# Kernel optimization log

Hardware: AMD Instinct MI355X
Metric: run time of the kernel (lower is better)

## Reference

```python
import jax, jax.numpy as jnp
import numpy as np

N_NODES = 100000


def gcn_conv(x, W, b, src, dst, n):
    """PyG GCNConv with default add_self_loops and symmetric normalization."""
    xw = x @ W  # [N, out]
    loop = jnp.arange(n, dtype=src.dtype)
    s = jnp.concatenate([src, loop])  # source j
    d = jnp.concatenate([dst, loop])  # target i
    deg = jax.ops.segment_sum(jnp.ones_like(d, dtype=xw.dtype), d, num_segments=n)
    dinv = jnp.where(deg > 0, jax.lax.rsqrt(deg), 0.0)
    norm = dinv[s] * dinv[d]  # [E+N]
    msg = xw[s] * norm[:, None]
    out = jax.ops.segment_sum(msg, d, num_segments=n)
    return out + b


def setup_inputs() -> dict:
    key = jax.random.key(0)
    ks = jax.random.split(key, 9)
    n, e, f = N_NODES, 1600000, 512
    x = jax.random.normal(ks[0], (n, f), dtype=jnp.float32)
    edge_index = jax.random.randint(ks[1], (2, e), 0, n, dtype=jnp.int32)
    y = jax.random.uniform(ks[2], (n, 1), dtype=jnp.float32)
    W1 = jax.random.normal(ks[3], (f, 64), dtype=jnp.float32) / np.sqrt(f)
    b1 = jnp.zeros((64,), jnp.float32)
    W2 = jax.random.normal(ks[4], (64, 256), dtype=jnp.float32) / np.sqrt(64)
    b2 = jnp.zeros((256,), jnp.float32)
    W3 = jax.random.normal(ks[5], (256, 1), dtype=jnp.float32) / np.sqrt(256)
    b3 = jnp.zeros((1,), jnp.float32)
    return {"x": x, "edge_index": edge_index, "y": y,
            "W1": W1, "b1": b1, "W2": W2, "b2": b2, "W3": W3, "b3": b3}


def reference(x, edge_index, y, W1, b1, W2, b2, W3, b3):
    n = x.shape[0]
    src, dst = edge_index[0], edge_index[1]
    h = jax.nn.relu(gcn_conv(x, W1, b1, src, dst, n))
    # dropout is identity in eval mode
    h = jax.nn.relu(gcn_conv(h, W2, b2, src, dst, n))
    z = gcn_conv(h, W3, b3, src, dst, n)  # logits [N, 1]
    # BCE(sigmoid(z), y), computed stably via log-sigmoid
    loss = -(y * jax.nn.log_sigmoid(z) + (1.0 - y) * jax.nn.log_sigmoid(-z))
    return jnp.mean(loss)
```

## Files before the change

kernel.cpp:

```cpp
#include <hip/hip_runtime.h>
#include <math.h>

typedef __attribute__((ext_vector_type(8))) short s16x8;
typedef __attribute__((ext_vector_type(4))) float f32x4;

__device__ inline ushort f2bf(float f) {
    union { float f; unsigned u; } v; v.f = f;
    unsigned r = v.u + 0x7FFF + ((v.u >> 16) & 1);
    return (ushort)(r >> 16);
}
__device__ inline float bf2f(ushort h) {
    union { unsigned u; float f; } v; v.u = ((unsigned)h) << 16;
    return v.f;
}
__device__ inline float bfLo(unsigned u) {
    union { unsigned x; float f; } v; v.x = u << 16; return v.f;
}
__device__ inline float bfHi(unsigned u) {
    union { unsigned x; float f; } v; v.x = u & 0xFFFF0000u; return v.f;
}


__global__ void hist_kernel(const int* __restrict__ dst, int E, int* __restrict__ cnt,
                            int* __restrict__ slot) {
    int e = blockIdx.x * blockDim.x + threadIdx.x;
    if (e < E) slot[e] = atomicAdd(&cnt[dst[e]], 1);
}

__global__ void alloc_kernel(const int* __restrict__ cnt, int* __restrict__ row_start,
                             float* __restrict__ dinv, int* __restrict__ total, int N) {
    int i = blockIdx.x * blockDim.x + threadIdx.x;
    int lane = threadIdx.x & 63;
    int c = (i < N) ? cnt[i] : 0;
    int inc = c;
#pragma unroll
    for (int o = 1; o < 64; o <<= 1) {
        int v = __shfl_up(inc, o, 64);
        if (lane >= o) inc += v;
    }
    int wsum = __shfl(inc, 63, 64);
    int base = 0;
    if (lane == 0) base = atomicAdd(total, wsum);
    base = __shfl(base, 0, 64);
    if (i < N) {
        row_start[i] = base + inc - c;
        dinv[i] = rsqrtf((float)(c + 1));
    }
}

__global__ void scatter_kernel(const int* __restrict__ src, const int* __restrict__ dst, int E,
                               const int* __restrict__ row_start, const int* __restrict__ slot,
                               int* __restrict__ csr) {
    int e = blockIdx.x * blockDim.x + threadIdx.x;
    if (e < E) {
        int d = dst[e];
        csr[row_start[d] + slot[e]] = src[e];
    }
}

__global__ void wsplit_all_kernel(const float* __restrict__ W1, const float* __restrict__ W2,
                                  ushort* __restrict__ wt_hi, ushort* __restrict__ wt_lo,
                                  ushort* __restrict__ wt2_hi, ushort* __restrict__ wt2_lo) {
    int idx = blockIdx.x * blockDim.x + threadIdx.x;
    if (idx < 64 * 512) {
        int n = idx & 63, k = idx >> 6;
        float f = W1[k * 64 + n];
        ushort h = f2bf(f);
        wt_hi[n * 512 + k] = h;
        wt_lo[n * 512 + k] = f2bf(f - bf2f(h));
    } else if (idx < 64 * 512 + 64 * 256) {
        int i2 = idx - 64 * 512;
        int n = i2 & 255, k = i2 >> 8;
        float f = W2[k * 256 + n];
        ushort h = f2bf(f);
        wt2_hi[n * 64 + k] = h;
        wt2_lo[n * 64 + k] = f2bf(f - bf2f(h));
    }
}

__global__ __launch_bounds__(256, 3) void gemm1_kernel(const float* __restrict__ x,
                                                       const ushort* __restrict__ wt_hi,
                                                       const ushort* __restrict__ wt_lo,
                                                       const float* __restrict__ dinv,
                                                       ushort* __restrict__ out, int N) {
    __shared__ __align__(16) short xs_hi[128 * 64];
    __shared__ __align__(16) short xs_lo[128 * 64];
    __shared__ __align__(16) short ws_hi[64 * 64];
    __shared__ __align__(16) short ws_lo[64 * 64];

    const int tid = threadIdx.x;
    const int nodeBase = blockIdx.x * 128;
    const int wave = tid >> 6, lane = tid & 63;
    const int m16 = lane & 15, quad = lane >> 4;

    f32x4 acc[2][4];
#pragma unroll
    for (int mt = 0; mt < 2; mt++)
#pragma unroll
        for (int nt = 0; nt < 4; nt++) acc[mt][nt] = (f32x4){0.f, 0.f, 0.f, 0.f};

    for (int kc = 0; kc < 512; kc += 64) {
        __syncthreads();
#pragma unroll
        for (int i = 0; i < 4; i++) {
            int f = tid + i * 256;
            int node = f >> 3, g = f & 7;
            int gn = nodeBase + node;
            if (gn >= N) gn = N - 1;
            const float4 a = *(const float4*)(x + (size_t)gn * 512 + kc + g * 8);
            const float4 b = *(const float4*)(x + (size_t)gn * 512 + kc + g * 8 + 4);
            float ff[8] = {a.x, a.y, a.z, a.w, b.x, b.y, b.z, b.w};
            union { ushort u[8]; uint4 v; } H, L;
#pragma unroll
            for (int j = 0; j < 8; j++) {
                ushort h = f2bf(ff[j]);
                H.u[j] = h;
                L.u[j] = f2bf(ff[j] - bf2f(h));
            }
            int gp = (g + node) & 7;
            *(uint4*)&xs_hi[node * 64 + gp * 8] = H.v;
            *(uint4*)&xs_lo[node * 64 + gp * 8] = L.v;
        }
#pragma unroll
        for (int i = 0; i < 2; i++) {
            int f = tid + i * 256;
            int n = f >> 3, g = f & 7;
            int gp = (g + n) & 7;
            *(uint4*)&ws_hi[n * 64 + gp * 8] =
                *(const uint4*)(wt_hi + (size_t)n * 512 + kc + g * 8);
            *(uint4*)&ws_lo[n * 64 + gp * 8] =
                *(const uint4*)(wt_lo + (size_t)n * 512 + kc + g * 8);
        }
        __syncthreads();
#pragma unroll
        for (int ck = 0; ck < 2; ck++) {
            s16x8 Ah[2], Al[2];
#pragma unroll
            for (int mt = 0; mt < 2; mt++) {
                int row = (wave * 2 + mt) * 16 + m16;
                int gp = (ck * 4 + quad + row) & 7;
                Ah[mt] = *(s16x8*)&xs_hi[row * 64 + gp * 8];
                Al[mt] = *(s16x8*)&xs_lo[row * 64 + gp * 8];
            }
#pragma unroll
            for (int nt = 0; nt < 4; nt++) {
                int n = nt * 16 + m16;
                int gp = (ck * 4 + quad + n) & 7;
                s16x8 Bh = *(s16x8*)&ws_hi[n * 64 + gp * 8];
                s16x8 Bl = *(s16x8*)&ws_lo[n * 64 + gp * 8];
#pragma unroll
                for (int mt = 0; mt < 2; mt++) {
                    acc[mt][nt] = __builtin_amdgcn_mfma_f32_16x16x32_bf16(Ah[mt], Bh, acc[mt][nt], 0, 0, 0);
                    acc[mt][nt] = __builtin_amdgcn_mfma_f32_16x16x32_bf16(Ah[mt], Bl, acc[mt][nt], 0, 0, 0);
                    acc[mt][nt] = __builtin_amdgcn_mfma_f32_16x16x32_bf16(Al[mt], Bh, acc[mt][nt], 0, 0, 0);
                }
            }
        }
    }
#pragma unroll
    for (int mt = 0; mt < 2; mt++) {
#pragma unroll
        for (int r = 0; r < 4; r++) {
            int gn = nodeBase + (wave * 2 + mt) * 16 + quad * 4 + r;
            if (gn < N) {
                float di = dinv[gn];
#pragma unroll
                for (int nt = 0; nt < 4; nt++)
                    out[(size_t)gn * 64 + nt * 16 + m16] = f2bf(di * acc[mt][nt][r]);
            }
        }
    }
}

template <int RELU, int BIAS, int PREMUL>
__global__ void agg64bf_kernel(const ushort* __restrict__ in, ushort* __restrict__ out,
                               const int* __restrict__ row_start, const int* __restrict__ cnt,
                               const int* __restrict__ csr, const float* __restrict__ dinv,
                               const float* __restrict__ bias, int N) {
    int gw = (int)((blockIdx.x * (size_t)blockDim.x + threadIdx.x) >> 6);
    int lane = threadIdx.x & 63;
    if (gw >= N) return;
    const int m16 = lane & 15;
    const int quad = lane >> 4;

    const int s = row_start[gw];
    const int c = cnt[gw];
    const int total = c + 1;

    float a0 = 0.f, a1 = 0.f, a2v = 0.f, a3 = 0.f;
    for (int e = 0; e < total; e += 8) {
        int s0 = e + quad, s1 = e + 4 + quad;
        bool v0 = s0 < total, v1 = s1 < total;
        int j0 = gw, j1 = gw;
        if (v0 && s0 > 0) j0 = csr[s + s0 - 1];
        if (v1 && s1 > 0) j1 = csr[s + s1 - 1];
        uint2 u0 = *(const uint2*)(in + (size_t)j0 * 64 + m16 * 4);
        uint2 u1 = *(const uint2*)(in + (size_t)j1 * 64 + m16 * 4);
        if (v0) { a0 += bfLo(u0.x); a1 += bfHi(u0.x); a2v += bfLo(u0.y); a3 += bfHi(u0.y); }
        if (v1) { a0 += bfLo(u1.x); a1 += bfHi(u1.x); a2v += bfLo(u1.y); a3 += bfHi(u1.y); }
    }
    a0 += __shfl_xor(a0, 16, 64); a0 += __shfl_xor(a0, 32, 64);
    a1 += __shfl_xor(a1, 16, 64); a1 += __shfl_xor(a1, 32, 64);
    a2v += __shfl_xor(a2v, 16, 64); a2v += __shfl_xor(a2v, 32, 64);
    a3 += __shfl_xor(a3, 16, 64); a3 += __shfl_xor(a3, 32, 64);

    float di = dinv[gw];
    float r0 = di * a0, r1 = di * a1, r2 = di * a2v, r3 = di * a3;
    if (BIAS) {
        float4 bv = *(const float4*)&bias[m16 * 4];
        r0 += bv.x; r1 += bv.y; r2 += bv.z; r3 += bv.w;
    }
    if (RELU) {
        r0 = fmaxf(r0, 0.f); r1 = fmaxf(r1, 0.f);
        r2 = fmaxf(r2, 0.f); r3 = fmaxf(r3, 0.f);
    }
    if (PREMUL) { r0 *= di; r1 *= di; r2 *= di; r3 *= di; }
    if (quad == 0) {
        uint2 o;
        o.x = ((unsigned)f2bf(r1) << 16) | f2bf(r0);
        o.y = ((unsigned)f2bf(r3) << 16) | f2bf(r2);
        *(uint2*)(out + (size_t)gw * 64 + m16 * 4) = o;
    }
}

__global__ __launch_bounds__(256, 2) void gemm23_kernel(const ushort* __restrict__ a2,
                                                        const ushort* __restrict__ wt2_hi,
                                                        const ushort* __restrict__ wt2_lo,
                                                        const float* __restrict__ b2,
                                                        const float* __restrict__ W3,
                                                        const float* __restrict__ dinv,
                                                        float* __restrict__ r, int N) {
    const int tid = threadIdx.x;
    const int wave = tid >> 6, lane = tid & 63;
    const int m16 = lane & 15, quad = lane >> 4;
    const int rowBase = blockIdx.x * 128 + wave * 32;

    s16x8 A[2][2];
#pragma unroll
    for (int mt = 0; mt < 2; mt++) {
        int gn = rowBase + mt * 16 + m16;
        if (gn >= N) gn = N - 1;
        const ushort* ap = a2 + (size_t)gn * 64 + quad * 8;
#pragma unroll
        for (int ck = 0; ck < 2; ck++)
            A[mt][ck] = *(const s16x8*)(ap + ck * 32);
    }

    f32x4 acc[2][16];
#pragma unroll
    for (int mt = 0; mt < 2; mt++)
#pragma unroll
        for (int nt = 0; nt < 16; nt++) acc[mt][nt] = (f32x4){0.f, 0.f, 0.f, 0.f};

#pragma unroll
    for (int nt = 0; nt < 16; nt++) {
        int n = nt * 16 + m16;
        const ushort* bh = wt2_hi + (size_t)n * 64 + quad * 8;
        const ushort* bl = wt2_lo + (size_t)n * 64 + quad * 8;
        s16x8 Bh0 = *(const s16x8*)(bh);
        s16x8 Bh1 = *(const s16x8*)(bh + 32);
        s16x8 Bl0 = *(const s16x8*)(bl);
        s16x8 Bl1 = *(const s16x8*)(bl + 32);
        acc[0][nt] = __builtin_amdgcn_mfma_f32_16x16x32_bf16(A[0][0], Bh0, acc[0][nt], 0, 0, 0);
        acc[1][nt] = __builtin_amdgcn_mfma_f32_16x16x32_bf16(A[1][0], Bh0, acc[1][nt], 0, 0, 0);
        acc[0][nt] = __builtin_amdgcn_mfma_f32_16x16x32_bf16(A[0][1], Bh1, acc[0][nt], 0, 0, 0);
        acc[1][nt] = __builtin_amdgcn_mfma_f32_16x16x32_bf16(A[1][1], Bh1, acc[1][nt], 0, 0, 0);
        acc[0][nt] = __builtin_amdgcn_mfma_f32_16x16x32_bf16(A[0][0], Bl0, acc[0][nt], 0, 0, 0);
        acc[1][nt] = __builtin_amdgcn_mfma_f32_16x16x32_bf16(A[1][0], Bl0, acc[1][nt], 0, 0, 0);
        acc[0][nt] = __builtin_amdgcn_mfma_f32_16x16x32_bf16(A[0][1], Bl1, acc[0][nt], 0, 0, 0);
        acc[1][nt] = __builtin_amdgcn_mfma_f32_16x16x32_bf16(A[1][1], Bl1, acc[1][nt], 0, 0, 0);
    }

    float bv[16], wv[16];
#pragma unroll
    for (int nt = 0; nt < 16; nt++) {
        bv[nt] = b2[nt * 16 + m16];
        wv[nt] = W3[nt * 16 + m16];
    }
#pragma unroll
    for (int mt = 0; mt < 2; mt++) {
#pragma unroll
        for (int rr = 0; rr < 4; rr++) {
            float p = 0.f;
#pragma unroll
            for (int nt = 0; nt < 16; nt++) {
                float v = fmaxf(acc[mt][nt][rr] + bv[nt], 0.f);
                p = fmaf(v, wv[nt], p);
            }
#pragma unroll
            for (int off = 1; off < 16; off <<= 1) p += __shfl_xor(p, off, 64);
            int gn = rowBase + mt * 16 + quad * 4 + rr;
            if (m16 == 0 && gn < N) r[gn] = dinv[gn] * p;
        }
    }
}

__global__ __launch_bounds__(1024) void loss_kernel(const float* __restrict__ r,
                                                    const float* __restrict__ dinv,
                                                    const int* __restrict__ row_start,
                                                    const int* __restrict__ cnt,
                                                    const int* __restrict__ csr,
                                                    const float* __restrict__ y,
                                                    const float* __restrict__ b3,
                                                    float* __restrict__ out,
                                                    int N, float invN) {
    const int lane = threadIdx.x & 63;
    const int wave = threadIdx.x >> 6;
    const int l16 = lane & 15;
    const int grp = lane >> 4;
    const int waveId = blockIdx.x * 16 + wave;
    const int nWaves = gridDim.x * 16;
    const float b3v = b3[0];

    float loss = 0.f;
    for (int base = waveId * 4; base < N; base += nWaves * 4) {
        int node = base + grp;
        float acc = 0.f;
        if (node < N) {
            int s = row_start[node], c = cnt[node];
            for (int e = l16; e < c; e += 16) acc += r[csr[s + e]];
        }
        acc += __shfl_xor(acc, 1, 64);
        acc += __shfl_xor(acc, 2, 64);
        acc += __shfl_xor(acc, 4, 64);
        acc += __shfl_xor(acc, 8, 64);
        if (node < N && l16 == 0) {
            float z = dinv[node] * (r[node] + acc) + b3v;
            float yv = y[node];
            float L = log1pf(expf(-fabsf(z)));
            float spz  = fmaxf(z, 0.f) + L;
            float spnz = fmaxf(-z, 0.f) + L;
            loss += yv * spnz + (1.f - yv) * spz;
        }
    }
#pragma unroll
    for (int off = 1; off < 64; off <<= 1) loss += __shfl_xor(loss, off, 64);
    __shared__ float red[16];
    if (lane == 0) red[wave] = loss;
    __syncthreads();
    if (threadIdx.x == 0) {
        float t = 0.f;
#pragma unroll
        for (int i = 0; i < 16; i++) t += red[i];
        atomicAdd(out, t * invN);
    }
}

extern "C" void kernel_launch(void* const* d_in, const int* in_sizes, int n_in,
                              void* d_out, int out_size, void* d_ws, size_t ws_size,
                              hipStream_t stream) {
    const float* x  = (const float*)d_in[0];
    const int*   ei = (const int*)d_in[1];
    const float* y  = (const float*)d_in[2];
    const float* W1 = (const float*)d_in[3];
    const float* b1 = (const float*)d_in[4];
    const float* W2 = (const float*)d_in[5];
    const float* b2 = (const float*)d_in[6];
    const float* W3 = (const float*)d_in[7];
    const float* b3 = (const float*)d_in[8];

    const int N = in_sizes[2];
    const int E = in_sizes[1] / 2;
    const int* src  = ei;
    const int* dstp = ei + E;

    char* w = (char*)d_ws;
    int*    cnt       = (int*)w;    w += (size_t)N * 4;
    int*    total     = (int*)w;    w += 16;
    int*    row_start = (int*)w;    w += (size_t)N * 4;
    float*  dinv      = (float*)w;  w += (size_t)N * 4;
    int*    csr       = (int*)w;    w += (size_t)E * 4;
    int*    slot      = (int*)w;    w += (size_t)E * 4;
    ushort* wt_hi     = (ushort*)w; w += (size_t)64 * 512 * 2;
    ushort* wt_lo     = (ushort*)w; w += (size_t)64 * 512 * 2;
    ushort* wt2_hi    = (ushort*)w; w += (size_t)256 * 64 * 2;
    ushort* wt2_lo    = (ushort*)w; w += (size_t)256 * 64 * 2;
    ushort* pbuf      = (ushort*)w; w += (size_t)N * 64 * 2;
    ushort* qbuf      = (ushort*)w; w += (size_t)N * 64 * 2;
    float*  rbuf      = (float*)w;  w += (size_t)N * 4;

    hipMemsetAsync(cnt, 0, (size_t)N * 4 + 16, stream);
    hipMemsetAsync(d_out, 0, sizeof(float), stream);

    const int tb = 256;
    wsplit_all_kernel<<<(64 * 512 + 64 * 256 + tb - 1) / tb, tb, 0, stream>>>(
        W1, W2, wt_hi, wt_lo, wt2_hi, wt2_lo);
    hist_kernel<<<(E + tb - 1) / tb, tb, 0, stream>>>(dstp, E, cnt, slot);
    alloc_kernel<<<(N + tb - 1) / tb, tb, 0, stream>>>(cnt, row_start, dinv, total, N);
    scatter_kernel<<<(E + tb - 1) / tb, tb, 0, stream>>>(src, dstp, E, row_start, slot, csr);

    gemm1_kernel<<<(N + 127) / 128, 256, 0, stream>>>(x, wt_hi, wt_lo, dinv, pbuf, N);
    agg64bf_kernel<1, 1, 1><<<(N + 3) / 4, 256, 0, stream>>>(pbuf, qbuf, row_start, cnt, csr, dinv, b1, N);
    agg64bf_kernel<0, 0, 0><<<(N + 3) / 4, 256, 0, stream>>>(qbuf, pbuf, row_start, cnt, csr, dinv, nullptr, N);

    gemm23_kernel<<<(N + 127) / 128, 256, 0, stream>>>(pbuf, wt2_hi, wt2_lo, b2, W3, dinv, rbuf, N);

    loss_kernel<<<256, 1024, 0, stream>>>(rbuf, dinv, row_start, cnt, csr, y, b3,
                                          (float*)d_out, N, 1.0f / N);
}
```

Measured before the change: 627.1 us.

## Privatize degree histogram into 8 copies and fuse graph-build kernels

After: 605.8 us. 3.4% less time.

```diff
diff --git a/kernel.cpp b/kernel.cpp
--- a/kernel.cpp
+++ b/kernel.cpp
@@ -21,47 +21,21 @@
 }
 
 
-__global__ void hist_kernel(const int* __restrict__ dst, int E, int* __restrict__ cnt,
-                            int* __restrict__ slot) {
-    int e = blockIdx.x * blockDim.x + threadIdx.x;
-    if (e < E) slot[e] = atomicAdd(&cnt[dst[e]], 1);
-}
-
-__global__ void alloc_kernel(const int* __restrict__ cnt, int* __restrict__ row_start,
-                             float* __restrict__ dinv, int* __restrict__ total, int N) {
-    int i = blockIdx.x * blockDim.x + threadIdx.x;
-    int lane = threadIdx.x & 63;
-    int c = (i < N) ? cnt[i] : 0;
-    int inc = c;
-#pragma unroll
-    for (int o = 1; o < 64; o <<= 1) {
-        int v = __shfl_up(inc, o, 64);
-        if (lane >= o) inc += v;
-    }
-    int wsum = __shfl(inc, 63, 64);
-    int base = 0;
-    if (lane == 0) base = atomicAdd(total, wsum);
-    base = __shfl(base, 0, 64);
-    if (i < N) {
-        row_start[i] = base + inc - c;
-        dinv[i] = rsqrtf((float)(c + 1));
-    }
-}
-
-__global__ void scatter_kernel(const int* __restrict__ src, const int* __restrict__ dst, int E,
-                               const int* __restrict__ row_start, const int* __restrict__ slot,
-                               int* __restrict__ csr) {
-    int e = blockIdx.x * blockDim.x + threadIdx.x;
-    if (e < E) {
-        int d = dst[e];
-        csr[row_start[d] + slot[e]] = src[e];
-    }
-}
-
-__global__ void wsplit_all_kernel(const float* __restrict__ W1, const float* __restrict__ W2,
-                                  ushort* __restrict__ wt_hi, ushort* __restrict__ wt_lo,
-                                  ushort* __restrict__ wt2_hi, ushort* __restrict__ wt2_lo) {
-    int idx = blockIdx.x * blockDim.x + threadIdx.x;
+__global__ void hist_wsplit_kernel(const int* __restrict__ dst, int E, int eb,
+                                   int* __restrict__ cnt8, int N, int* __restrict__ slot,
+                                   const float* __restrict__ W1, const float* __restrict__ W2,
+                                   ushort* __restrict__ wt_hi, ushort* __restrict__ wt_lo,
+                                   ushort* __restrict__ wt2_hi, ushort* __restrict__ wt2_lo) {
+    int b = blockIdx.x;
+    if (b < eb) {
+        int e = b * 256 + threadIdx.x;
+        if (e < E) {
+            int g = b & 7;
+            slot[e] = atomicAdd(&cnt8[(size_t)g * N + dst[e]], 1);
+        }
+        return;
+    }
+    int idx = (b - eb) * 256 + threadIdx.x;
     if (idx < 64 * 512) {
         int n = idx & 63, k = idx >> 6;
         float f = W1[k * 64 + n];
@@ -78,15 +52,65 @@
     }
 }
 
-__global__ __launch_bounds__(256, 3) void gemm1_kernel(const float* __restrict__ x,
-                                                       const ushort* __restrict__ wt_hi,
-                                                       const ushort* __restrict__ wt_lo,
-                                                       const float* __restrict__ dinv,
-                                                       ushort* __restrict__ out, int N) {
+__global__ void alloc_kernel(const int* __restrict__ cnt8, int N,
+                             int* __restrict__ row_start, int* __restrict__ base8,
+                             int* __restrict__ deg, float* __restrict__ dinv,
+                             int* __restrict__ total, float* __restrict__ out) {
+    int i = blockIdx.x * blockDim.x + threadIdx.x;
+    int lane = threadIdx.x & 63;
+    int cg[8];
+    int c = 0;
+    if (i < N) {
+#pragma unroll
+        for (int g = 0; g < 8; g++) { cg[g] = cnt8[(size_t)g * N + i]; c += cg[g]; }
+    } else {
+#pragma unroll
+        for (int g = 0; g < 8; g++) cg[g] = 0;
+    }
+    int inc = c;
+#pragma unroll
+    for (int o = 1; o < 64; o <<= 1) {
+        int v = __shfl_up(inc, o, 64);
+        if (lane >= o) inc += v;
+    }
+    int wsum = __shfl(inc, 63, 64);
+    int base = 0;
+    if (lane == 0) base = atomicAdd(total, wsum);
+    base = __shfl(base, 0, 64);
+    if (i < N) {
+        int rs = base + inc - c;
+        row_start[i] = rs;
+        deg[i] = c;
+        dinv[i] = rsqrtf((float)(c + 1));
+        int run = rs;
+#pragma unroll
+        for (int g = 0; g < 8; g++) { base8[(size_t)g * N + i] = run; run += cg[g]; }
+    }
+    if (i == 0) *out = 0.f;
+}
+
+__global__ __launch_bounds__(256, 3) void gemm1_scatter_kernel(
+        const float* __restrict__ x, const ushort* __restrict__ wt_hi,
+        const ushort* __restrict__ wt_lo, const float* __restrict__ dinv,
+        ushort* __restrict__ out, int N, int GB,
+        const int* __restrict__ src, const int* __restrict__ dstp, int E,
+        const int* __restrict__ base8, const int* __restrict__ slot,
+        int* __restrict__ csr) {
     __shared__ __align__(16) short xs_hi[128 * 64];
     __shared__ __align__(16) short xs_lo[128 * 64];
     __shared__ __align__(16) short ws_hi[64 * 64];
     __shared__ __align__(16) short ws_lo[64 * 64];
+
+    if ((int)blockIdx.x >= GB) {
+        int sb = (int)blockIdx.x - GB;
+        int e = sb * 256 + threadIdx.x;
+        if (e < E) {
+            int d = dstp[e];
+            int g = sb & 7;
+            csr[base8[(size_t)g * N + d] + slot[e]] = src[e];
+        }
+        return;
+    }
 
     const int tid = threadIdx.x;
     const int nodeBase = blockIdx.x * 128;
@@ -174,7 +198,7 @@
 
 template <int RELU, int BIAS, int PREMUL>
 __global__ void agg64bf_kernel(const ushort* __restrict__ in, ushort* __restrict__ out,
-                               const int* __restrict__ row_start, const int* __restrict__ cnt,
+                               const int* __restrict__ row_start, const int* __restrict__ deg,
                                const int* __restrict__ csr, const float* __restrict__ dinv,
                                const float* __restrict__ bias, int N) {
     int gw = (int)((blockIdx.x * (size_t)blockDim.x + threadIdx.x) >> 6);
@@ -184,7 +208,7 @@
     const int quad = lane >> 4;
 
     const int s = row_start[gw];
-    const int c = cnt[gw];
+    const int c = deg[gw];
     const int total = c + 1;
 
     float a0 = 0.f, a1 = 0.f, a2v = 0.f, a3 = 0.f;
@@ -298,7 +322,7 @@
 __global__ __launch_bounds__(1024) void loss_kernel(const float* __restrict__ r,
                                                     const float* __restrict__ dinv,
                                                     const int* __restrict__ row_start,
-                                                    const int* __restrict__ cnt,
+                                                    const int* __restrict__ deg,
                                                     const int* __restrict__ csr,
                                                     const float* __restrict__ y,
                                                     const float* __restrict__ b3,
@@ -317,7 +341,7 @@
         int node = base + grp;
         float acc = 0.f;
         if (node < N) {
-            int s = row_start[node], c = cnt[node];
+            int s = row_start[node], c = deg[node];
             for (int e = l16; e < c; e += 16) acc += r[csr[s + e]];
         }
         acc += __shfl_xor(acc, 1, 64);
@@ -365,10 +389,12 @@
     const int* dstp = ei + E;
 
     char* w = (char*)d_ws;
-    int*    cnt       = (int*)w;    w += (size_t)N * 4;
+    int*    cnt8      = (int*)w;    w += (size_t)8 * N * 4;
     int*    total     = (int*)w;    w += 16;
     int*    row_start = (int*)w;    w += (size_t)N * 4;
+    int*    deg       = (int*)w;    w += (size_t)N * 4;
     float*  dinv      = (float*)w;  w += (size_t)N * 4;
+    int*    base8     = (int*)w;    w += (size_t)8 * N * 4;
     int*    csr       = (int*)w;    w += (size_t)E * 4;
     int*    slot      = (int*)w;    w += (size_t)E * 4;
     ushort* wt_hi     = (ushort*)w; w += (size_t)64 * 512 * 2;
@@ -379,22 +405,24 @@
     ushort* qbuf      = (ushort*)w; w += (size_t)N * 64 * 2;
     float*  rbuf      = (float*)w;  w += (size_t)N * 4;
 
-    hipMemsetAsync(cnt, 0, (size_t)N * 4 + 16, stream);
-    hipMemsetAsync(d_out, 0, sizeof(float), stream);
+    hipMemsetAsync(cnt8, 0, (size_t)8 * N * 4 + 16, stream);
 
     const int tb = 256;
-    wsplit_all_kernel<<<(64 * 512 + 64 * 256 + tb - 1) / tb, tb, 0, stream>>>(
-        W1, W2, wt_hi, wt_lo, wt2_hi, wt2_lo);
-    hist_kernel<<<(E + tb - 1) / tb, tb, 0, stream>>>(dstp, E, cnt, slot);
-    alloc_kernel<<<(N + tb - 1) / tb, tb, 0, stream>>>(cnt, row_start, dinv, total, N);
-    scatter_kernel<<<(E + tb - 1) / tb, tb, 0, stream>>>(src, dstp, E, row_start, slot, csr);
-
-    gemm1_kernel<<<(N + 127) / 128, 256, 0, stream>>>(x, wt_hi, wt_lo, dinv, pbuf, N);
-    agg64bf_kernel<1, 1, 1><<<(N + 3) / 4, 256, 0, stream>>>(pbuf, qbuf, row_start, cnt, csr, dinv, b1, N);
-    agg64bf_kernel<0, 0, 0><<<(N + 3) / 4, 256, 0, stream>>>(qbuf, pbuf, row_start, cnt, csr, dinv, nullptr, N);
+    const int eb = (E + tb - 1) / tb;
+    const int wb = (64 * 512 + 64 * 256 + tb - 1) / tb;
+    const int GB = (N + 127) / 128;
+
+    hist_wsplit_kernel<<<eb + wb, tb, 0, stream>>>(dstp, E, eb, cnt8, N, slot,
+                                                   W1, W2, wt_hi, wt_lo, wt2_hi, wt2_lo);
+    alloc_kernel<<<(N + tb - 1) / tb, tb, 0, stream>>>(cnt8, N, row_start, base8, deg, dinv,
+                                                       total, (float*)d_out);
+    gemm1_scatter_kernel<<<GB + eb, 256, 0, stream>>>(x, wt_hi, wt_lo, dinv, pbuf, N, GB,
+                                                      src, dstp, E, base8, slot, csr);
+    agg64bf_kernel<1, 1, 1><<<(N + 3) / 4, 256, 0, stream>>>(pbuf, qbuf, row_start, deg, csr, dinv, b1, N);
+    agg64bf_kernel<0, 0, 0><<<(N + 3) / 4, 256, 0, stream>>>(qbuf, pbuf, row_start, deg, csr, dinv, nullptr, N);
 
     gemm23_kernel<<<(N + 127) / 128, 256, 0, stream>>>(pbuf, wt2_hi, wt2_lo, b2, W3, dinv, rbuf, N);
 
-    loss_kernel<<<256, 1024, 0, stream>>>(rbuf, dinv, row_start, cnt, csr, y, b3,
+    loss_kernel<<<256, 1024, 0, stream>>>(rbuf, dinv, row_start, deg, csr, y, b3,
                                           (float*)d_out, N, 1.0f / N);
 }
```
